# Kernel tuning notes

Measured on AMD Instinct MI355X. Metric: run time of the kernel, lower is better.

## Reference

```python
import jax, jax.numpy as jnp
import numpy as np

BUCKET_BINS = np.array([0, 1, 2, 3, 4, 5, 7, 8, 15, 16, 31, 32, 63, 64], dtype=np.int32)
MAX_WINDOW = 8  # args.span_maximum_length


def _span_index_table(L):
    # Static enumeration of all spans of width 1..MAX_WINDOW (stride-1 unfold).
    starts, ends = [], []
    for w in range(1, min(L, MAX_WINDOW) + 1):
        s = np.arange(0, L - w + 1)
        starts.append(s)
        ends.append(s + w)
    return (np.concatenate(starts).astype(np.int32),
            np.concatenate(ends).astype(np.int32))


def _bucket(width):
    # index of last bin with width >= bin value
    return jnp.searchsorted(jnp.asarray(BUCKET_BINS), width, side='right') - 1


def _fnn(h, W1, b1, W2, b2, W3, b3):
    # Linear->ReLU->(Dropout: eval identity)->Linear->ReLU->Linear->Softmax
    h = jax.nn.relu(h @ W1 + b1)
    h = jax.nn.relu(h @ W2 + b2)
    return jax.nn.softmax(h @ W3 + b3, axis=-1)


def setup_inputs() -> dict:
    key = jax.random.key(0)
    ks = jax.random.split(key, 16)
    B, L, D = 8, 256, 768
    H, WD, DD = 1024, 25, 25
    span_dim = 2 * D + WD          # 1561
    pair_dim = 2 * span_dim + DD   # 3147
    f = jnp.float32

    def g(k, shape, scale):
        return jax.random.normal(k, shape, dtype=f) * scale

    return {
        'x': g(ks[0], (B, L, D), 1.0),
        'width_emb': g(ks[1], (len(BUCKET_BINS), WD), 0.02),
        'dist_emb': g(ks[2], (len(BUCKET_BINS), DD), 0.02),
        'Ws1': g(ks[3], (span_dim, H), 0.02), 'bs1': jnp.zeros((H,), f),
        'Ws2': g(ks[4], (H, H), 0.02), 'bs2': jnp.zeros((H,), f),
        'Ws3': g(ks[5], (H, 3), 0.02), 'bs3': jnp.zeros((3,), f),
        'Wp1': g(ks[6], (pair_dim, H), 0.02), 'bp1': jnp.zeros((H,), f),
        'Wp2': g(ks[7], (H, H), 0.02), 'bp2': jnp.zeros((H,), f),
        'Wp3': g(ks[8], (H, 4), 0.02), 'bp3': jnp.zeros((4,), f),
        'nz': 64,
    }


def reference(x, width_emb, dist_emb, Ws1, bs1, Ws2, bs2, Ws3, bs3,
              Wp1, bp1, Wp2, bp2, Wp3, bp3, nz):
    B, L, D = x.shape
    starts_np, ends_np = _span_index_table(L)
    starts = jnp.asarray(starts_np)
    ends = jnp.asarray(ends_np)

    # ---- SpanRepresentation: [start token, end token, width bucket emb] ----
    w_emb = width_emb[_bucket(ends - starts)]                     # [S, WD]
    spans = jnp.concatenate([
        x[:, starts_np, :],                                       # [B,S,D]
        x[:, ends_np - 1, :],                                     # [B,S,D]
        jnp.broadcast_to(w_emb, (B,) + w_emb.shape),              # [B,S,WD]
    ], axis=-1)                                                   # [B,S,span_dim]

    # ---- span_fnn + PrunedTargetOpinion (top-k on aspect/opinion probs) ----
    span_prob = _fnn(spans, Ws1, bs1, Ws2, bs2, Ws3, bs3)         # [B,S,3]
    _, t_idx = jax.lax.top_k(span_prob[:, :, 1], nz)              # aspect  [B,nz]
    _, o_idx = jax.lax.top_k(span_prob[:, :, 2], nz)              # opinion [B,nz]

    # ---- PairRepresentation: all target x opinion pairs ----
    t_rep = jnp.take_along_axis(spans, t_idx[:, :, None], axis=1) # [B,nz,sd]
    o_rep = jnp.take_along_axis(spans, o_idx[:, :, None], axis=1)
    ta, tb = starts[t_idx], ends[t_idx]                           # [B,nz]
    oc, od = starts[o_idx], ends[o_idx]
    # min_distance(a,b,c,d) = min(|b-c|, |a-d|)
    dist = jnp.minimum(jnp.abs(tb[:, :, None] - oc[:, None, :]),
                       jnp.abs(ta[:, :, None] - od[:, None, :]))  # [B,nz,nz]
    d_emb = dist_emb[_bucket(dist)]                               # [B,nz,nz,DD]
    sd = spans.shape[-1]
    pairs = jnp.concatenate([
        jnp.broadcast_to(t_rep[:, :, None, :], (B, nz, nz, sd)),
        jnp.broadcast_to(o_rep[:, None, :, :], (B, nz, nz, sd)),
        d_emb,
    ], axis=-1).reshape(B, nz * nz, 2 * sd + d_emb.shape[-1])     # [B,nz^2,pair_dim]

    pair_prob = _fnn(pairs, Wp1, bp1, Wp2, bp2, Wp3, bp3)         # [B,nz^2,4]
    return span_prob, pair_prob
```

## Files before the change

### kernel.cpp

```cpp
#include <hip/hip_runtime.h>
#include <cstdint>
#include <cstddef>

#define BATCH 8
#define SEQ   256
#define DIM   768
#define NSPAN 2020
#define HID   1024
#define NZ    64

typedef unsigned short u16;
typedef unsigned int   u32;
typedef unsigned long long u64;

typedef __bf16 bf16x8 __attribute__((ext_vector_type(8)));
typedef float  f32x4  __attribute__((ext_vector_type(4)));

__device__ __forceinline__ u16 f2bf(float f) {
    union { float f; u32 u; } x; x.f = f;
    u32 r = x.u + 0x7fffu + ((x.u >> 16) & 1u);
    return (u16)(r >> 16);
}
__device__ __forceinline__ float bf2f(u16 b) {
    union { u32 u; float f; } x; x.u = ((u32)b) << 16;
// ... 58 lines not shown
    }
    if (bid < 6296) {
        int t = bid - 6144;
        int row = t >> 2;
        int h = (t & 3) * 256 + tid;
        const int wb[8] = {1,2,3,4,5,5,6,7};
        if (row < 8) {
            int bk = wb[row];
            float acc = bs1[h];
            for (int j = 0; j < 25; ++j) acc = fmaf(wemb[bk*25+j], Ws1[(size_t)(1536+j)*HID + h], acc);
            wtabS[row*HID + h] = acc;
        } else if (row < 16) {
            int bk = wb[row-8];
            float acc = 0.f;
            for (int j = 0; j < 25; ++j) acc = fmaf(wemb[bk*25+j], Wp1[(size_t)(1536+j)*HID + h], acc);
            wtabPt[(row-8)*HID + h] = acc;
        } else if (row < 24) {
            int bk = wb[row-16];
            float acc = 0.f;
            for (int j = 0; j < 25; ++j) acc = fmaf(wemb[bk*25+j], Wp1[(size_t)(3097+j)*HID + h], acc);
            wtabPo[(row-16)*HID + h] = acc;
        } else {
            int tt = row - 24;
            float acc = bp1[h];
            for (int j = 0; j < 25; ++j) acc = fmaf(demb[tt*25+j], Wp1[(size_t)(3122+j)*HID + h], acc);
            dtab[tt*HID + h] = acc;
        }
        return;
    }
    const int tb = bid - 6296;
    const int tr = tid >> 3;
    const int tc4 = (tid & 7) * 4;
    int job, tk, tn, blk = 0;
    if (tb < 1536)      { job = 0; tk = tb % 24; tn = tb / 24; }
    else if (tb < 2560) { job = 1; int t = tb - 1536; tk = t & 31; tn = t >> 5; }
    else if (tb < 3584) { job = 2; int t = tb - 2560; tk = t & 31; tn = t >> 5; }
    else                { job = 3; int t = tb - 3584; blk = t / 768; int r = t - blk * 768; tk = r % 24; tn = r / 24; }
    const int k0 = tk * 32, n0 = tn * 32;

    int k = k0 + tr;
    float4 v;
    if (job == 0) {
        const float* s = (n0 < 1024) ? (Ws1 + (size_t)k * HID + n0)
                                     : (Ws1 + (size_t)(768 + k) * HID + (n0 - 1024));
        v = *(const float4*)(s + tc4);
    } else if (job == 1) {
        v = *(const float4*)(Ws2 + (size_t)k * HID + n0 + tc4);
    } else if (job == 2) {
        v = *(const float4*)(Wp2 + (size_t)k * HID + n0 + tc4);
    } else {
        const int roff[4] = {0, 768, 1561, 2329};
        v = *(const float4*)(Wp1 + (size_t)(roff[blk] + k) * HID + n0 + tc4);
    }
    tile[tr][tc4+0] = v.x; tile[tr][tc4+1] = v.y;
    tile[tr][tc4+2] = v.z; tile[tr][tc4+3] = v.w;
    __syncthreads();

    int nn = n0 + tr;
    float w0 = tile[tc4+0][tr], w1 = tile[tc4+1][tr];
    float w2 = tile[tc4+2][tr], w3 = tile[tc4+3][tr];
    if (job == 0) {
        size_t d = (size_t)nn * 768 + k0 + tc4;
        u16 h0,l0,h1,l1,h2,l2,h3,l3;
        splitbf(w0,h0,l0); splitbf(w1,h1,l1); splitbf(w2,h2,l2); splitbf(w3,h3,l3);
        *(uint2*)(W1Th + d) = make_uint2((u32)h0 | ((u32)h1 << 16), (u32)h2 | ((u32)h3 << 16));
        *(uint2*)(W1Tl + d) = make_uint2((u32)l0 | ((u32)l1 << 16), (u32)l2 | ((u32)l3 << 16));
    } else if (job == 1) {
        size_t d = (size_t)nn * 1024 + k0 + tc4;
        u16 h0,l0,h1,l1,h2,l2,h3,l3;
        splitbf(w0,h0,l0); splitbf(w1,h1,l1); splitbf(w2,h2,l2); splitbf(w3,h3,l3);
        *(uint2*)(W2Th + d) = make_uint2((u32)h0 | ((u32)h1 << 16), (u32)h2 | ((u32)h3 << 16));
        *(uint2*)(W2Tl + d) = make_uint2((u32)l0 | ((u32)l1 << 16), (u32)l2 | ((u32)l3 << 16));
    } else if (job == 2) {
        size_t d = (size_t)nn * 1024 + k0 + tc4;
        *(uint2*)(Wp2T + d) = make_uint2((u32)f2bf(w0) | ((u32)f2bf(w1) << 16),
                                         (u32)f2bf(w2) | ((u32)f2bf(w3) << 16));
    } else {
        size_t d = (size_t)blk * 786432 + (size_t)nn * 768 + k0 + tc4;
        *(uint2*)(Wp1T4 + d) = make_uint2((u32)f2bf(w0) | ((u32)f2bf(w1) << 16),
                                          (u32)f2bf(w2) | ((u32)f2bf(w3) << 16));
    }
}

__global__ __launch_bounds__(256) void k_gemm3bf(
    const u16* __restrict__ Ah, const u16* __restrict__ Al, int lda,
    const u16* __restrict__ BTh, const u16* __restrict__ BTl, int ldb,
    float* __restrict__ C, int ldc,
    int M, int K, int nby, int sft)
{
    int bx, by;
    xcd_map(blockIdx.x, sft, bx, by);
    if (by >= nby) return;
    __shared__ __align__(16) u16 sm[2 * 16384];
    const int tid = threadIdx.x;
    const int bm = by * 128, bn = bx * 128;
    const int wave = tid >> 6, lane = tid & 63;
    const int wr = wave >> 1, wc = wave & 1;
    const int q = lane >> 4, tl = lane & 15;

    f32x4 zero = {0.f, 0.f, 0.f, 0.f};
    f32x4 acc[4][4];
#pragma unroll
    for (int i = 0; i < 4; ++i)
#pragma unroll
        for (int j = 0; j < 4; ++j) acc[i][j] = zero;

    const int srow = lane >> 2;
    const int scol = (lane & 3) * 8;
    int ra0 = bm + wave * 32 + srow;      if (ra0 >= M) ra0 = M - 1;
    int ra1 = bm + wave * 32 + 16 + srow; if (ra1 >= M) ra1 = M - 1;
    const int rb0 = bn + wave * 32 + srow;
    const int rb1 = bn + wave * 32 + 16 + srow;
    const u32 oA0 = wave * 1024,          oA1 = oA0 + 512;
    const u32 oL0 = 4096 + wave * 1024,   oL1 = oL0 + 512;
    const u32 oB0 = 8192 + wave * 1024,   oB1 = oB0 + 512;
    const u32 oC0 = 12288 + wave * 1024,  oC1 = oC0 + 512;
    const u16* gA0 = Ah  + (size_t)ra0 * lda + scol;
    const u16* gA1 = Ah  + (size_t)ra1 * lda + scol;
    const u16* gL0 = Al  + (size_t)ra0 * lda + scol;
    const u16* gL1 = Al  + (size_t)ra1 * lda + scol;
    const u16* gB0 = BTh + (size_t)rb0 * ldb + scol;
    const u16* gB1 = BTh + (size_t)rb1 * ldb + scol;
    const u16* gC0 = BTl + (size_t)rb0 * ldb + scol;
    const u16* gC1 = BTl + (size_t)rb1 * ldb + scol;

    gld_lds16(gA0, sm + oA0); gld_lds16(gA1, sm + oA1);
    gld_lds16(gL0, sm + oL0); gld_lds16(gL1, sm + oL1);
    gld_lds16(gB0, sm + oB0); gld_lds16(gB1, sm + oB1);
    gld_lds16(gC0, sm + oC0); gld_lds16(gC1, sm + oC1);
    asm volatile("s_waitcnt vmcnt(0)" ::: "memory");
    asm volatile("s_barrier" ::: "memory");

    const int NT = K >> 5;
    for (int kt = 0; kt < NT; ++kt) {
        const u16* smr = sm + ((kt & 1) ? 16384u : 0u);
        u16*       smw = sm + ((kt & 1) ? 0u : 16384u);
        if (kt < NT - 1) {
            const int k0 = (kt + 1) * 32;
            gld_lds16(gA0 + k0, smw + oA0); gld_lds16(gA1 + k0, smw + oA1);
            gld_lds16(gL0 + k0, smw + oL0); gld_lds16(gL1 + k0, smw + oL1);
            gld_lds16(gB0 + k0, smw + oB0); gld_lds16(gB1 + k0, smw + oB1);
            gld_lds16(gC0 + k0, smw + oC0); gld_lds16(gC1 + k0, smw + oC1);
            asm volatile("s_waitcnt vmcnt(8)" ::: "memory");
        } else {
            asm volatile("s_waitcnt vmcnt(0)" ::: "memory");
        }
        asm volatile("s_barrier" ::: "memory");
        bf16x8 ah[4], al[4], bh[4], bl[4];
#pragma unroll
        for (int t = 0; t < 4; ++t) {
            int arow = (wr*64 + t*16 + tl) * 32 + q*8;
            int brow = (wc*64 + t*16 + tl) * 32 + q*8;
            ah[t] = *(const bf16x8*)(smr + arow);
            al[t] = *(const bf16x8*)(smr + 4096 + arow);
            bh[t] = *(const bf16x8*)(smr + 8192 + brow);
            bl[t] = *(const bf16x8*)(smr + 12288 + brow);
        }
#pragma unroll
        for (int ti = 0; ti < 4; ++ti)
#pragma unroll
            for (int tj = 0; tj < 4; ++tj) {
                acc[ti][tj] = __builtin_amdgcn_mfma_f32_16x16x32_bf16(ah[ti], bh[tj], acc[ti][tj], 0, 0, 0);
                acc[ti][tj] = __builtin_amdgcn_mfma_f32_16x16x32_bf16(al[ti], bh[tj], acc[ti][tj], 0, 0, 0);
                acc[ti][tj] = __builtin_amdgcn_mfma_f32_16x16x32_bf16(ah[ti], bl[tj], acc[ti][tj], 0, 0, 0);
            }
        asm volatile("s_barrier" ::: "memory");
    }
#pragma unroll
    for (int ti = 0; ti < 4; ++ti) {
#pragma unroll
        for (int tj = 0; tj < 4; ++tj) {
            int gcol = bn + wc*64 + tj*16 + tl;
#pragma unroll
            for (int r = 0; r < 4; ++r) {
                int grow = bm + wr*64 + ti*16 + q*4 + r;
                if (grow >= M) continue;
                C[(size_t)grow * ldc + gcol] = acc[ti][tj][r];
            }
        }
    }
}

#define MFB __builtin_amdgcn_mfma_f32_16x16x32_bf16
#define MFROW(i, A, B) \
    acc[i][0] = MFB(A, B[0], acc[i][0], 0, 0, 0); \
    acc[i][1] = MFB(A, B[1], acc[i][1], 0, 0, 0); \
    acc[i][2] = MFB(A, B[2], acc[i][2], 0, 0, 0); \
    acc[i][3] = MFB(A, B[3], acc[i][3], 0, 0, 0);

__global__ __launch_bounds__(512, 2) void k_span_l2(
    const u16* __restrict__ Ah, const u16* __restrict__ Al,
    const u16* __restrict__ BTh, const u16* __restrict__ BTl,
    const float* __restrict__ bs2, const float* __restrict__ Ws3,
    float* __restrict__ part, int M)
{
    __shared__ __align__(16) u16 sm[65536];
    const int tid = threadIdx.x;
    const int swz = (blockIdx.x & 7) * 32 + (blockIdx.x >> 3);
    const int by = swz >> 2, bx = swz & 3;
    const int bm = by * 256, bn = bx * 256;
    const int wave = tid >> 6, lane = tid & 63;
    const int wm = wave >> 2, wn = wave & 3;
    const int tl = lane & 15, q8 = lane >> 4;

    const int sr  = lane >> 2;
    const int scs = lane & 3;
    const int scl = scs ^ ((sr >> 1) & 3);
    const u16* gsrc[8];
    u32 ldst[8];
#pragma unroll
    for (int c = 0; c < 4; ++c) {
        int arr  = 2 + (c >> 1);
        int half = c & 1;
        int sb   = wave;
        int row  = bn + half * 128 + sb * 16 + sr;
        const u16* base = (arr == 2) ? BTh : BTl;
        gsrc[c] = base + (size_t)row * HID + scl * 8;
        ldst[c] = arr * 8192 + half * 4096 + sb * 512;
    }
#pragma unroll
    for (int p = 0; p < 4; ++p) {
        int arr  = wave >> 2;
        int half = (wave >> 1) & 1;
        int sb   = 2 * p + (wave & 1);
        int row  = bm + half * 128 + sb * 16 + sr;
        if (row >= M) row = M - 1;
        const u16* base = arr ? Al : Ah;
        gsrc[4 + p] = base + (size_t)row * HID + scl * 8;
        ldst[4 + p] = arr * 8192 + half * 4096 + sb * 512;
    }
    const int cpr = q8 ^ ((tl >> 1) & 3);
    const u32 lof = (u32)(tl * 32 + cpr * 8);
    const u32 rA  = (u32)(wm * 4096) + lof;
    const u32 rB  = 16384u + (u32)((wn >> 1) * 4096 + (wn & 1) * 2048) + lof;

    f32x4 zero = {0.f, 0.f, 0.f, 0.f};
    f32x4 acc[8][4];
#pragma unroll
    for (int i = 0; i < 8; ++i)
#pragma unroll
        for (int j = 0; j < 4; ++j) acc[i][j] = zero;

#pragma unroll
    for (int c = 0; c < 8; ++c) gld_lds16(gsrc[c], sm + ldst[c]);
    asm volatile("s_waitcnt vmcnt(3)" ::: "memory");
    asm volatile("s_barrier" ::: "memory");

    bf16x8 bh[4], bl[4];
    bf16x8 aXh0, aXh1, aXl0, aXl1, aYh0, aYh1, aYl0, aYl1;
#pragma unroll
    for (int fn = 0; fn < 4; ++fn) {
        bh[fn] = *(const bf16x8*)(sm + rB + fn * 512);
        bl[fn] = *(const bf16x8*)(sm + rB + 8192 + fn * 512);
    }
    aXh0 = *(const bf16x8*)(sm + rA + 0 * 512);
    aXh1 = *(const bf16x8*)(sm + rA + 1 * 512);
    aXl0 = *(const bf16x8*)(sm + rA + 8192 + 0 * 512);
    aXl1 = *(const bf16x8*)(sm + rA + 8192 + 1 * 512);

    for (int t = 0; t < 32; ++t) {
        const u16* smr = sm + ((t & 1) ? 32768u : 0u);
        u16*       smw = sm + ((t & 1) ? 0u : 32768u);
        const int  kn  = (t + 1) * 32;
        gld_lds16(gsrc[0] + kn, smw + ldst[0]);
        gld_lds16(gsrc[1] + kn, smw + ldst[1]);
        gld_lds16(gsrc[2] + kn, smw + ldst[2]);
        asm volatile("s_waitcnt vmcnt(5)" ::: "memory");
        asm volatile("s_barrier" ::: "memory");
        __builtin_amdgcn_sched_barrier(0);
        __builtin_amdgcn_s_setprio(1);
        MFROW(0, aXh0, bh) MFROW(1, aXh1, bh)
        aYh0 = *(const bf16x8*)(smr + rA + 2 * 512);
        aYh1 = *(const bf16x8*)(smr + rA + 3 * 512);
        aYl0 = *(const bf16x8*)(smr + rA + 8192 + 2 * 512);
        aYl1 = *(const bf16x8*)(smr + rA + 8192 + 3 * 512);
        MFROW(0, aXl0, bh) MFROW(1, aXl1, bh)
        MFROW(0, aXh0, bl) MFROW(1, aXh1, bl)
        __builtin_amdgcn_s_setprio(0);
        gld_lds16(gsrc[3] + kn, smw + ldst[3]);
        gld_lds16(gsrc[4] + kn, smw + ldst[4]);
        asm volatile("s_waitcnt vmcnt(6)" ::: "memory");
        asm volatile("s_barrier" ::: "memory");
        __builtin_amdgcn_sched_barrier(0);
        __builtin_amdgcn_s_setprio(1);
        MFROW(2, aYh0, bh) MFROW(3, aYh1, bh)
        aXh0 = *(const bf16x8*)(smr + rA + 4 * 512);
        aXh1 = *(const bf16x8*)(smr + rA + 5 * 512);
        aXl0 = *(const bf16x8*)(smr + rA + 8192 + 4 * 512);
        aXl1 = *(const bf16x8*)(smr + rA + 8192 + 5 * 512);
        MFROW(2, aYl0, bh) MFROW(3, aYl1, bh)
        MFROW(2, aYh0, bl) MFROW(3, aYh1, bl)
        __builtin_amdgcn_s_setprio(0);
        gld_lds16(gsrc[5] + kn, smw + ldst[5]);
        gld_lds16(gsrc[6] + kn, smw + ldst[6]);
        asm volatile("s_waitcnt vmcnt(7)" ::: "memory");
        asm volatile("s_barrier" ::: "memory");
        __builtin_amdgcn_sched_barrier(0);
        __builtin_amdgcn_s_setprio(1);
        MFROW(4, aXh0, bh) MFROW(5, aXh1, bh)
        aYh0 = *(const bf16x8*)(smr + rA + 6 * 512);
        aYh1 = *(const bf16x8*)(smr + rA + 7 * 512);
        aYl0 = *(const bf16x8*)(smr + rA + 8192 + 6 * 512);
        aYl1 = *(const bf16x8*)(smr + rA + 8192 + 7 * 512);
        MFROW(4, aXl0, bh) MFROW(5, aXl1, bh)
        MFROW(4, aXh0, bl) MFROW(5, aXh1, bl)
        __builtin_amdgcn_s_setprio(0);
        gld_lds16(gsrc[7] + kn, smw + ldst[7]);
        asm volatile("s_waitcnt vmcnt(3)" ::: "memory");
        asm volatile("s_barrier" ::: "memory");
        __builtin_amdgcn_sched_barrier(0);
        __builtin_amdgcn_s_setprio(1);
        MFROW(6, aYh0, bh) MFROW(7, aYh1, bh)
        aXh0 = *(const bf16x8*)(smw + rA + 0 * 512);
        aXh1 = *(const bf16x8*)(smw + rA + 1 * 512);
        aXl0 = *(const bf16x8*)(smw + rA + 8192 + 0 * 512);
        aXl1 = *(const bf16x8*)(smw + rA + 8192 + 1 * 512);
        MFROW(6, aYl0, bh) MFROW(7, aYl1, bh)
        MFROW(6, aYh0, bl) MFROW(7, aYh1, bl)
        __builtin_amdgcn_s_setprio(0);
#pragma unroll
        for (int fn = 0; fn < 4; ++fn) {
            bh[fn] = *(const bf16x8*)(smw + rB + fn * 512);
            bl[fn] = *(const bf16x8*)(smw + rB + 8192 + fn * 512);
        }
        asm volatile("s_barrier" ::: "memory");
    }

    const int slot = bx * 4 + wn;
#pragma unroll
    for (int fm = 0; fm < 8; ++fm) {
#pragma unroll
        for (int r = 0; r < 4; ++r) {
            int grow = bm + wm * 128 + fm * 16 + q8 * 4 + r;
            float l0 = 0.f, l1 = 0.f, l2 = 0.f;
#pragma unroll
            for (int fn = 0; fn < 4; ++fn) {
                int gcol = bn + wn * 64 + fn * 16 + tl;
                float v = fmaxf(acc[fm][fn][r] + bs2[gcol], 0.f);
                const float* w3 = Ws3 + gcol * 3;
                l0 = fmaf(v, w3[0], l0);
                l1 = fmaf(v, w3[1], l1);
                l2 = fmaf(v, w3[2], l2);
            }
#pragma unroll
            for (int off = 8; off > 0; off >>= 1) {
                l0 += __shfl_down(l0, off, 16);
                l1 += __shfl_down(l1, off, 16);
                l2 += __shfl_down(l2, off, 16);
            }
            if (tl == 0 && grow < M) {
                float* dst = part + ((size_t)grow * 16 + slot) * 3;
                dst[0] = l0; dst[1] = l1; dst[2] = l2;
            }
        }
    }
    asm volatile("s_waitcnt vmcnt(0)" ::: "memory");
}

__global__ __launch_bounds__(256) void k_pairL1(
    const u16* __restrict__ xh, const u16* __restrict__ Wp1T4,
    float* __restrict__ TO2, const int* __restrict__ toks)
{
    __shared__ __align__(16) u16 sm[2 * 4096];
    const int tid = threadIdx.x;
    const int bid = blockIdx.x;
    const int p = bid >> 8;
    const int bx = bid & 15, by = (bid >> 4) & 15;
    const int bm = by * 64, bn = bx * 64;
    const int wave = tid >> 6, lane = tid & 63;
    const int wr = wave >> 1, wc = wave & 1;
    const int q = lane >> 4, tl = lane & 15;
    const bool isO = bm >= 512;

    f32x4 zero = {0.f, 0.f, 0.f, 0.f};
    f32x4 acc[2][2];
#pragma unroll
    for (int i = 0; i < 2; ++i)
#pragma unroll
        for (int j = 0; j < 2; ++j) acc[i][j] = zero;

    const int srow = tid >> 2;
    const int scol = (tid & 3) * 8;
    const u32 oA = wave * 512;
    const u32 oB = 2048 + wave * 512;

    int arow = toks[bm + srow + p * 1024];
    const u16* gA = xh + (size_t)arow * DIM + scol;
    const u16* gB = Wp1T4 + ((size_t)((isO ? 2 : 0) + p) * 1024 + bn + srow) * DIM + scol;

    gld_lds16(gA, sm + oA);
    gld_lds16(gB, sm + oB);
    asm volatile("s_waitcnt vmcnt(0)" ::: "memory");
    asm volatile("s_barrier" ::: "memory");

    const int NT = DIM / 32;
    for (int kt = 0; kt < NT; ++kt) {
        const u16* smr = sm + ((kt & 1) ? 4096u : 0u);
        u16*       smw = sm + ((kt & 1) ? 0u : 4096u);
        if (kt < NT - 1) {
            const int k0 = (kt + 1) * 32;
            gld_lds16(gA + k0, smw + oA);
            gld_lds16(gB + k0, smw + oB);
// ... 106 lines not shown
    if (tid < NZ) {
        u64 key = keys[tid];
        int fi = (int)(0xFFFFFFFFu - (u32)(key & 0xFFFFFFFFu));
        if (fi < 0 || fi >= NSPAN) fi = 0;
        outp[tid] = fi;
        int st, en, w; span_decode(fi, st, en, w);
        int base = (head == 1 ? 0 : 512) + b * NZ + tid;
        toks[base] = b * SEQ + st;
        toks[1024 + base] = b * SEQ + en - 1;
    }
}

__global__ __launch_bounds__(256) void k_build_h1p(
    const float* __restrict__ TO2, const int* __restrict__ t_idx, const int* __restrict__ o_idx,
    const float* __restrict__ wtabPt, const float* __restrict__ wtabPo,
    const float* __restrict__ dtab, u16* __restrict__ h1p)
{
    __shared__ float Ts[8][HID];
    __shared__ float Os[4][HID];
    const int bid = blockIdx.x;
    const int b = bid >> 7;
    const int it = (bid >> 4) & 7;
    const int jt = bid & 15;
    const int i0 = it * 8, j0 = jt * 4;
    const int tid = threadIdx.x;
    const int k4 = tid * 4;
    const size_t PS = (size_t)1024 * HID;

    int tinfo[8][2];
    int oinfo[4][2];
#pragma unroll
    for (int r = 0; r < 8; ++r) {
        int i = i0 + r;
        int ts = t_idx[b*64 + i];
        int ta, tb, wt; span_decode(ts, ta, tb, wt);
        tinfo[r][0] = ta; tinfo[r][1] = tb;
        float4 t0 = *(const float4*)(TO2 + (size_t)(b*64 + i) * HID + k4);
        float4 t1 = *(const float4*)(TO2 + PS + (size_t)(b*64 + i) * HID + k4);
        float4 pp = *(const float4*)(wtabPt + (size_t)(wt-1) * HID + k4);
        Ts[r][k4+0] = t0.x + t1.x + pp.x;
        Ts[r][k4+1] = t0.y + t1.y + pp.y;
        Ts[r][k4+2] = t0.z + t1.z + pp.z;
        Ts[r][k4+3] = t0.w + t1.w + pp.w;
    }
#pragma unroll
    for (int r = 0; r < 4; ++r) {
        int j = j0 + r;
        int os = o_idx[b*64 + j];
        int oc, od, wo; span_decode(os, oc, od, wo);
        oinfo[r][0] = oc; oinfo[r][1] = od;
        float4 o0 = *(const float4*)(TO2 + (size_t)(512 + b*64 + j) * HID + k4);
        float4 o1 = *(const float4*)(TO2 + PS + (size_t)(512 + b*64 + j) * HID + k4);
        float4 qq = *(const float4*)(wtabPo + (size_t)(wo-1) * HID + k4);
        Os[r][k4+0] = o0.x + o1.x + qq.x;
        Os[r][k4+1] = o0.y + o1.y + qq.y;
        Os[r][k4+2] = o0.z + o1.z + qq.z;
        Os[r][k4+3] = o0.w + o1.w + qq.w;
    }
    __syncthreads();

#pragma unroll
    for (int ri = 0; ri < 8; ++ri) {
#pragma unroll
        for (int rj = 0; rj < 4; ++rj) {
            int ta = tinfo[ri][0], tb = tinfo[ri][1];
            int oc = oinfo[rj][0], od = oinfo[rj][1];
            int d1 = tb - oc; d1 = d1 < 0 ? -d1 : d1;
            int d2 = ta - od; d2 = d2 < 0 ? -d2 : d2;
            int dist = d1 < d2 ? d1 : d2;
            int db = dbucket(dist);
            const float4 dd = *(const float4*)(dtab + (size_t)db * HID + k4);
            float vx = fmaxf(Ts[ri][k4+0] + Os[rj][k4+0] + dd.x, 0.f);
            float vy = fmaxf(Ts[ri][k4+1] + Os[rj][k4+1] + dd.y, 0.f);
            float vz = fmaxf(Ts[ri][k4+2] + Os[rj][k4+2] + dd.z, 0.f);
            float vw = fmaxf(Ts[ri][k4+3] + Os[rj][k4+3] + dd.w, 0.f);
            u32 p0 = (u32)f2bf(vx) | ((u32)f2bf(vy) << 16);
            u32 p1 = (u32)f2bf(vz) | ((u32)f2bf(vw) << 16);
            int row = b * 4096 + (i0 + ri) * 64 + (j0 + rj);
            *(uint2*)(h1p + (size_t)row * HID + k4) = make_uint2(p0, p1);
        }
    }
}

__global__ __launch_bounds__(512, 2) void k_pair_l2(
    const u16* __restrict__ Abf, const u16* __restrict__ BT,
    const float* __restrict__ bp2, const float* __restrict__ Wp3,
    float* __restrict__ part)
{
    __shared__ __align__(16) u16 sm[65536];
    const int tid = threadIdx.x;
    const int swz = (blockIdx.x & 7) * 64 + (blockIdx.x >> 3);
    const int by = swz >> 2, bx = swz & 3;
    const int bm = by * 256, bn = bx * 256;
    const int wave = tid >> 6, lane = tid & 63;
    const int wm = wave >> 2, wn = wave & 3;
    const int tl = lane & 15, q8 = lane >> 4;

    const int sr  = lane >> 2;
    const int scs = lane & 3;
    const int scl = scs ^ ((sr >> 1) & 3);
    const u16* gsrc[8];
    u32 ldst[8];
#pragma unroll
    for (int c = 0; c < 4; ++c) {
        int half = c >> 1;
        int sb   = (c & 1) * 8 + wave;
        int row  = bn + half * 128 + (sb >> 1) * 16 + sr;
        gsrc[c] = BT + (size_t)row * HID + (sb & 1) * 32 + scl * 8;
        ldst[c] = 16384 + half * 8192 + sb * 512;
    }
#pragma unroll
    for (int p = 0; p < 4; ++p) {
        int half = wave >> 2;
        int sb   = 4 * p + (wave & 3);
        int row  = bm + half * 128 + (sb >> 1) * 16 + sr;
        gsrc[4 + p] = Abf + (size_t)row * HID + (sb & 1) * 32 + scl * 8;
        ldst[4 + p] = half * 8192 + sb * 512;
    }
    const int cpr = q8 ^ ((tl >> 1) & 3);
    const u32 lof = (u32)(tl * 32 + cpr * 8);
    const u32 rA  = (u32)(wm * 8192) + lof;
    const u32 rB  = 16384u + (u32)((wn >> 1) * 8192 + (wn & 1) * 4096) + lof;

    f32x4 zero = {0.f, 0.f, 0.f, 0.f};
    f32x4 acc[8][4];
#pragma unroll
    for (int i = 0; i < 8; ++i)
#pragma unroll
        for (int j = 0; j < 4; ++j) acc[i][j] = zero;

#pragma unroll
    for (int c = 0; c < 8; ++c) gld_lds16(gsrc[c], sm + ldst[c]);
    asm volatile("s_waitcnt vmcnt(3)" ::: "memory");
    asm volatile("s_barrier" ::: "memory");

    bf16x8 b0[4], b1[4];
    bf16x8 xa00, xa01, xa10, xa11, ya00, ya01, ya10, ya11;
#pragma unroll
    for (int fn = 0; fn < 4; ++fn) {
        b0[fn] = *(const bf16x8*)(sm + rB + (fn * 2 + 0) * 512);
        b1[fn] = *(const bf16x8*)(sm + rB + (fn * 2 + 1) * 512);
    }
    xa00 = *(const bf16x8*)(sm + rA + 0 * 512);
    xa01 = *(const bf16x8*)(sm + rA + 1 * 512);
    xa10 = *(const bf16x8*)(sm + rA + 2 * 512);
    xa11 = *(const bf16x8*)(sm + rA + 3 * 512);

    for (int t = 0; t < 16; ++t) {
        const u16* smr = sm + ((t & 1) ? 32768u : 0u);
        u16*       smw = sm + ((t & 1) ? 0u : 32768u);
        const int  kn  = (t + 1) * 64;
        gld_lds16(gsrc[0] + kn, smw + ldst[0]);
        gld_lds16(gsrc[1] + kn, smw + ldst[1]);
        gld_lds16(gsrc[2] + kn, smw + ldst[2]);
        asm volatile("s_waitcnt vmcnt(5)" ::: "memory");
        asm volatile("s_barrier" ::: "memory");
        __builtin_amdgcn_sched_barrier(0);
        __builtin_amdgcn_s_setprio(1);
        MFROW(0, xa00, b0) MFROW(1, xa10, b0)
        ya00 = *(const bf16x8*)(smr + rA + 4 * 512);
        ya01 = *(const bf16x8*)(smr + rA + 5 * 512);
        ya10 = *(const bf16x8*)(smr + rA + 6 * 512);
        ya11 = *(const bf16x8*)(smr + rA + 7 * 512);
        MFROW(0, xa01, b1) MFROW(1, xa11, b1)
        __builtin_amdgcn_s_setprio(0);
        gld_lds16(gsrc[3] + kn, smw + ldst[3]);
        gld_lds16(gsrc[4] + kn, smw + ldst[4]);
        asm volatile("s_waitcnt vmcnt(6)" ::: "memory");
        asm volatile("s_barrier" ::: "memory");
        __builtin_amdgcn_sched_barrier(0);
        __builtin_amdgcn_s_setprio(1);
        MFROW(2, ya00, b0) MFROW(3, ya10, b0)
        xa00 = *(const bf16x8*)(smr + rA + 8 * 512);
        xa01 = *(const bf16x8*)(smr + rA + 9 * 512);
        xa10 = *(const bf16x8*)(smr + rA + 10 * 512);
        xa11 = *(const bf16x8*)(smr + rA + 11 * 512);
        MFROW(2, ya01, b1) MFROW(3, ya11, b1)
        __builtin_amdgcn_s_setprio(0);
        gld_lds16(gsrc[5] + kn, smw + ldst[5]);
        gld_lds16(gsrc[6] + kn, smw + ldst[6]);
        asm volatile("s_waitcnt vmcnt(7)" ::: "memory");
        asm volatile("s_barrier" ::: "memory");
        __builtin_amdgcn_sched_barrier(0);
        __builtin_amdgcn_s_setprio(1);
        MFROW(4, xa00, b0) MFROW(5, xa10, b0)
        ya00 = *(const bf16x8*)(smr + rA + 12 * 512);
        ya01 = *(const bf16x8*)(smr + rA + 13 * 512);
        ya10 = *(const bf16x8*)(smr + rA + 14 * 512);
        ya11 = *(const bf16x8*)(smr + rA + 15 * 512);
        MFROW(4, xa01, b1) MFROW(5, xa11, b1)
        __builtin_amdgcn_s_setprio(0);
        gld_lds16(gsrc[7] + kn, smw + ldst[7]);
        asm volatile("s_waitcnt vmcnt(3)" ::: "memory");
        asm volatile("s_barrier" ::: "memory");
        __builtin_amdgcn_sched_barrier(0);
        __builtin_amdgcn_s_setprio(1);
        MFROW(6, ya00, b0) MFROW(7, ya10, b0)
        xa00 = *(const bf16x8*)(smw + rA + 0 * 512);
        xa01 = *(const bf16x8*)(smw + rA + 1 * 512);
        xa10 = *(const bf16x8*)(smw + rA + 2 * 512);
        xa11 = *(const bf16x8*)(smw + rA + 3 * 512);
        MFROW(6, ya01, b1) MFROW(7, ya11, b1)
        __builtin_amdgcn_s_setprio(0);
#pragma unroll
        for (int fn = 0; fn < 4; ++fn) {
            b0[fn] = *(const bf16x8*)(smw + rB + (fn * 2 + 0) * 512);
            b1[fn] = *(const bf16x8*)(smw + rB + (fn * 2 + 1) * 512);
        }
        asm volatile("s_barrier" ::: "memory");
    }

    const int slot = bx * 4 + wn;
#pragma unroll
    for (int fm = 0; fm < 8; ++fm) {
#pragma unroll
        for (int r = 0; r < 4; ++r) {
            int grow = bm + wm * 128 + fm * 16 + q8 * 4 + r;
            float l0 = 0.f, l1 = 0.f, l2 = 0.f, l3 = 0.f;
#pragma unroll
            for (int fn = 0; fn < 4; ++fn) {
                int gcol = bn + wn * 64 + fn * 16 + tl;
                float v = fmaxf(acc[fm][fn][r] + bp2[gcol], 0.f);
                const float4 w = *(const float4*)(Wp3 + gcol * 4);
                l0 = fmaf(v, w.x, l0); l1 = fmaf(v, w.y, l1);
                l2 = fmaf(v, w.z, l2); l3 = fmaf(v, w.w, l3);
            }
#pragma unroll
            for (int off = 8; off > 0; off >>= 1) {
                l0 += __shfl_down(l0, off, 16);
                l1 += __shfl_down(l1, off, 16);
                l2 += __shfl_down(l2, off, 16);
                l3 += __shfl_down(l3, off, 16);
            }
            if (tl == 0) {
                float* dst = part + ((size_t)grow * 16 + slot) * 4;
                dst[0] = l0; dst[1] = l1; dst[2] = l2; dst[3] = l3;
            }
        }
    }
    asm volatile("s_waitcnt vmcnt(0)" ::: "memory");
}

__global__ __launch_bounds__(256) void k_pair_red(
    const float* __restrict__ part, const float* __restrict__ bp3,
    float* __restrict__ out)
{
    int r = blockIdx.x * 256 + threadIdx.x;
    const float4* p = (const float4*)(part + (size_t)r * 64);
    float s0 = bp3[0], s1 = bp3[1], s2 = bp3[2], s3 = bp3[3];
#pragma unroll
    for (int t = 0; t < 16; ++t) {
        float4 v = p[t];
        s0 += v.x; s1 += v.y; s2 += v.z; s3 += v.w;
    }
    float m = fmaxf(fmaxf(s0, s1), fmaxf(s2, s3));
    float e0 = expf(s0 - m), e1 = expf(s1 - m), e2 = expf(s2 - m), e3 = expf(s3 - m);
    float inv = 1.f / (e0 + e1 + e2 + e3);
    float* o = out + (size_t)r * 4;
    o[0] = e0 * inv; o[1] = e1 * inv; o[2] = e2 * inv; o[3] = e3 * inv;
}

extern "C" void kernel_launch(void* const* d_in, const int* in_sizes, int n_in,
                              void* d_out, int out_size, void* d_ws, size_t ws_size,
                              hipStream_t stream)
{
    const float* x    = (const float*)d_in[0];
    const float* wemb = (const float*)d_in[1];
    const float* demb = (const float*)d_in[2];
    const float* Ws1  = (const float*)d_in[3];
    const float* bs1  = (const float*)d_in[4];
    const float* Ws2  = (const float*)d_in[5];
    const float* bs2  = (const float*)d_in[6];
    const float* Ws3  = (const float*)d_in[7];
    const float* bs3  = (const float*)d_in[8];
    const float* Wp1  = (const float*)d_in[9];
    const float* bp1  = (const float*)d_in[10];
    const float* Wp2  = (const float*)d_in[11];
    const float* bp2  = (const float*)d_in[12];
    const float* Wp3  = (const float*)d_in[13];
    const float* bp3  = (const float*)d_in[14];
    float* out = (float*)d_out;
    char* ws = (char*)d_ws;

    const size_t RSZ = (size_t)32768 * HID * 2;
    size_t off = 0;
    auto alloc = [&](size_t bytes) -> void* {
        void* p = ws + off;
        off += (bytes + 255) & ~(size_t)255;
        return p;
    };
    char* R1 = (char*)alloc(RSZ);
    char* R2 = (char*)alloc(RSZ);
    u16*   h1h  = (u16*)R1;
    u16*   h1l  = (u16*)(R1 + (size_t)16160 * HID * 2);
    float* XALL = (float*)R2;
    u16*   xl   = (u16*)(R2 + (16u << 20));
    u16*   W1Th = (u16*)(R2 + (19u << 20));
    u16*   W1Tl = (u16*)(R2 + (22u << 20));
    u16*   h1p  = (u16*)R2;
    u16*   xh     = (u16*)alloc((size_t)2048 * DIM * 2);
    float* TO2    = (float*)alloc((size_t)2 * 1024 * HID * 4);
    float* partS  = (float*)alloc((size_t)16160 * 16 * 3 * 4);
    float* partP  = (float*)alloc((size_t)32768 * 16 * 4 * 4);
    u16*   W2Th   = (u16*)alloc((size_t)1024 * 1024 * 2);
    u16*   W2Tl   = (u16*)alloc((size_t)1024 * 1024 * 2);
    u16*   Wp2T   = (u16*)alloc((size_t)1024 * 1024 * 2);
    u16*   Wp1T4  = (u16*)alloc((size_t)4 * 1024 * 768 * 2);
    float* wtabS  = (float*)alloc(8 * HID * 4);
    float* wtabPt = (float*)alloc(8 * HID * 4);
    float* wtabPo = (float*)alloc(8 * HID * 4);
    float* dtab   = (float*)alloc(14 * HID * 4);
    int*   t_idx  = (int*)alloc(BATCH * NZ * 4);
    int*   o_idx  = (int*)alloc(BATCH * NZ * 4);
    int*   toks   = (int*)alloc(2048 * 4);
    (void)ws_size; (void)in_sizes; (void)n_in; (void)out_size;

    k_prep<<<12952, 256, 0, stream>>>(x, xh, xl, wemb, demb, bs1, bp1,
                                      wtabS, wtabPt, wtabPo, dtab,
                                      Ws1, W1Th, W1Tl, Ws2, W2Th, W2Tl,
                                      Wp2, Wp2T, Wp1, Wp1T4);

    k_gemm3bf<<<256, 256, 0, stream>>>(xh, xl, 768, W1Th, W1Tl, 768,
                                       XALL, 2048, 2048, 768, 16, 4);
    k_build_h1s<<<16160, 256, 0, stream>>>(XALL, wtabS, h1h, h1l);
    k_span_l2<<<256, 512, 0, stream>>>(h1h, h1l, W2Th, W2Tl, bs2, Ws3, partS, 16160);
    k_topk<<<16, 1024, 0, stream>>>(partS, bs3, out, t_idx, o_idx, toks);
    k_pairL1<<<512, 256, 0, stream>>>(xh, Wp1T4, TO2, toks);
    k_build_h1p<<<1024, 256, 0, stream>>>(TO2, t_idx, o_idx, wtabPt, wtabPo, dtab, h1p);
    k_pair_l2<<<512, 512, 0, stream>>>(h1p, Wp2T, bp2, Wp3, partP);
    k_pair_red<<<128, 256, 0, stream>>>(partP, bp3, out + 48480);
}
```

Before: 457.6 us.

## Rework GEMM kernels: 8-wave gemm3bf with swizzled LDS, restructured l2 pipelines

k_gemm3bf moves from 4 to 8 waves per block, with each wave owning a 64x32 output tile. Global-to-LDS loads are split by array across wave pairs and use an XOR-swizzled column layout to cut LDS bank conflicts. In k_span_l2, the A-fragment LDS reads now come after all MFMAs of a phase instead of being interleaved with them, fenced by sched barriers. In k_pair_l2, the hand-unrolled register double-buffered phases become a macro that loads fragments at the start of each phase and adds an extra barrier, trading load/compute overlap for lower register pressure and simpler code.

```diff
diff --git a/kernel.cpp b/kernel.cpp
--- a/kernel.cpp
+++ b/kernel.cpp
@@ -164,7 +164,14 @@
     }
 }
 
-__global__ __launch_bounds__(256) void k_gemm3bf(
+#define MFB __builtin_amdgcn_mfma_f32_16x16x32_bf16
+#define MFROW(i, A, B) \
+    acc[i][0] = MFB(A, B[0], acc[i][0], 0, 0, 0); \
+    acc[i][1] = MFB(A, B[1], acc[i][1], 0, 0, 0); \
+    acc[i][2] = MFB(A, B[2], acc[i][2], 0, 0, 0); \
+    acc[i][3] = MFB(A, B[3], acc[i][3], 0, 0, 0);
+
+__global__ __launch_bounds__(512) void k_gemm3bf(
     const u16* __restrict__ Ah, const u16* __restrict__ Al, int lda,
     const u16* __restrict__ BTh, const u16* __restrict__ BTl, int ldb,
     float* __restrict__ C, int ldc,
@@ -177,39 +184,37 @@
     const int tid = threadIdx.x;
     const int bm = by * 128, bn = bx * 128;
     const int wave = tid >> 6, lane = tid & 63;
-    const int wr = wave >> 1, wc = wave & 1;
-    const int q = lane >> 4, tl = lane & 15;
+    const int wr = wave >> 2, wc = wave & 3;
+    const int q8 = lane >> 4, tl = lane & 15;
 
     f32x4 zero = {0.f, 0.f, 0.f, 0.f};
-    f32x4 acc[4][4];
+    f32x4 acc[4][2];
 #pragma unroll
     for (int i = 0; i < 4; ++i)
 #pragma unroll
-        for (int j = 0; j < 4; ++j) acc[i][j] = zero;
-
-    const int srow = lane >> 2;
-    const int scol = (lane & 3) * 8;
-    int ra0 = bm + wave * 32 + srow;      if (ra0 >= M) ra0 = M - 1;
-    int ra1 = bm + wave * 32 + 16 + srow; if (ra1 >= M) ra1 = M - 1;
-    const int rb0 = bn + wave * 32 + srow;
-    const int rb1 = bn + wave * 32 + 16 + srow;
-    const u32 oA0 = wave * 1024,          oA1 = oA0 + 512;
-    const u32 oL0 = 4096 + wave * 1024,   oL1 = oL0 + 512;
-    const u32 oB0 = 8192 + wave * 1024,   oB1 = oB0 + 512;
-    const u32 oC0 = 12288 + wave * 1024,  oC1 = oC0 + 512;
-    const u16* gA0 = Ah  + (size_t)ra0 * lda + scol;
-    const u16* gA1 = Ah  + (size_t)ra1 * lda + scol;
-    const u16* gL0 = Al  + (size_t)ra0 * lda + scol;
-    const u16* gL1 = Al  + (size_t)ra1 * lda + scol;
-    const u16* gB0 = BTh + (size_t)rb0 * ldb + scol;
-    const u16* gB1 = BTh + (size_t)rb1 * ldb + scol;
-    const u16* gC0 = BTl + (size_t)rb0 * ldb + scol;
-    const u16* gC1 = BTl + (size_t)rb1 * ldb + scol;
-
-    gld_lds16(gA0, sm + oA0); gld_lds16(gA1, sm + oA1);
-    gld_lds16(gL0, sm + oL0); gld_lds16(gL1, sm + oL1);
-    gld_lds16(gB0, sm + oB0); gld_lds16(gB1, sm + oB1);
-    gld_lds16(gC0, sm + oC0); gld_lds16(gC1, sm + oC1);
+        for (int j = 0; j < 2; ++j) acc[i][j] = zero;
+
+    const int arr  = wave >> 1;
+    const int half = wave & 1;
+    const int sr   = lane >> 2;
+    const int scs  = lane & 3;
+    const int scl  = scs ^ ((sr >> 1) & 3);
+    const u16* gsrc[4];
+    u32 ldst[4];
+#pragma unroll
+    for (int j = 0; j < 4; ++j) {
+        int row = ((arr < 2) ? bm : bn) + half * 64 + j * 16 + sr;
+        if (arr < 2 && row >= M) row = M - 1;
+        const u16* base = (arr == 0) ? Ah : (arr == 1) ? Al : (arr == 2) ? BTh : BTl;
+        int ld = (arr < 2) ? lda : ldb;
+        gsrc[j] = base + (size_t)row * ld + scl * 8;
+        ldst[j] = arr * 4096 + half * 2048 + j * 512;
+    }
+    const int cpr = q8 ^ ((tl >> 1) & 3);
+    const u32 lof = (u32)(tl * 32 + cpr * 8);
+
+#pragma unroll
+    for (int j = 0; j < 4; ++j) gld_lds16(gsrc[j], sm + ldst[j]);
     asm volatile("s_waitcnt vmcnt(0)" ::: "memory");
     asm volatile("s_barrier" ::: "memory");
 
@@ -219,56 +224,49 @@
         u16*       smw = sm + ((kt & 1) ? 0u : 16384u);
         if (kt < NT - 1) {
             const int k0 = (kt + 1) * 32;
-            gld_lds16(gA0 + k0, smw + oA0); gld_lds16(gA1 + k0, smw + oA1);
-            gld_lds16(gL0 + k0, smw + oL0); gld_lds16(gL1 + k0, smw + oL1);
-            gld_lds16(gB0 + k0, smw + oB0); gld_lds16(gB1 + k0, smw + oB1);
-            gld_lds16(gC0 + k0, smw + oC0); gld_lds16(gC1 + k0, smw + oC1);
-            asm volatile("s_waitcnt vmcnt(8)" ::: "memory");
+#pragma unroll
+            for (int j = 0; j < 4; ++j) gld_lds16(gsrc[j] + k0, smw + ldst[j]);
+            asm volatile("s_waitcnt vmcnt(4)" ::: "memory");
         } else {
             asm volatile("s_waitcnt vmcnt(0)" ::: "memory");
         }
         asm volatile("s_barrier" ::: "memory");
-        bf16x8 ah[4], al[4], bh[4], bl[4];
-#pragma unroll
-        for (int t = 0; t < 4; ++t) {
-            int arow = (wr*64 + t*16 + tl) * 32 + q*8;
-            int brow = (wc*64 + t*16 + tl) * 32 + q*8;
-            ah[t] = *(const bf16x8*)(smr + arow);
-            al[t] = *(const bf16x8*)(smr + 4096 + arow);
-            bh[t] = *(const bf16x8*)(smr + 8192 + brow);
-            bl[t] = *(const bf16x8*)(smr + 12288 + brow);
-        }
-#pragma unroll
-        for (int ti = 0; ti < 4; ++ti)
-#pragma unroll
-            for (int tj = 0; tj < 4; ++tj) {
-                acc[ti][tj] = __builtin_amdgcn_mfma_f32_16x16x32_bf16(ah[ti], bh[tj], acc[ti][tj], 0, 0, 0);
-                acc[ti][tj] = __builtin_amdgcn_mfma_f32_16x16x32_bf16(al[ti], bh[tj], acc[ti][tj], 0, 0, 0);
-                acc[ti][tj] = __builtin_amdgcn_mfma_f32_16x16x32_bf16(ah[ti], bl[tj], acc[ti][tj], 0, 0, 0);
+        __builtin_amdgcn_sched_barrier(0);
+        bf16x8 ah[4], al[4], bh[2], bl[2];
+#pragma unroll
+        for (int fm = 0; fm < 4; ++fm) {
+            ah[fm] = *(const bf16x8*)(smr + (wr*4 + fm) * 512 + lof);
+            al[fm] = *(const bf16x8*)(smr + 4096 + (wr*4 + fm) * 512 + lof);
+        }
+#pragma unroll
+        for (int fn = 0; fn < 2; ++fn) {
+            bh[fn] = *(const bf16x8*)(smr + 8192 + (wc*2 + fn) * 512 + lof);
+            bl[fn] = *(const bf16x8*)(smr + 12288 + (wc*2 + fn) * 512 + lof);
+        }
+#pragma unroll
+        for (int fm = 0; fm < 4; ++fm)
+#pragma unroll
+            for (int fn = 0; fn < 2; ++fn) {
+                acc[fm][fn] = MFB(ah[fm], bh[fn], acc[fm][fn], 0, 0, 0);
+                acc[fm][fn] = MFB(al[fm], bh[fn], acc[fm][fn], 0, 0, 0);
+                acc[fm][fn] = MFB(ah[fm], bl[fn], acc[fm][fn], 0, 0, 0);
             }
         asm volatile("s_barrier" ::: "memory");
     }
 #pragma unroll
-    for (int ti = 0; ti < 4; ++ti) {
-#pragma unroll
-        for (int tj = 0; tj < 4; ++tj) {
-            int gcol = bn + wc*64 + tj*16 + tl;
+    for (int fm = 0; fm < 4; ++fm) {
+#pragma unroll
+        for (int fn = 0; fn < 2; ++fn) {
+            int gcol = bn + wc*32 + fn*16 + tl;
 #pragma unroll
             for (int r = 0; r < 4; ++r) {
-                int grow = bm + wr*64 + ti*16 + q*4 + r;
+                int grow = bm + wr*64 + fm*16 + q8*4 + r;
                 if (grow >= M) continue;
-                C[(size_t)grow * ldc + gcol] = acc[ti][tj][r];
-            }
-        }
-    }
-}
-
-#define MFB __builtin_amdgcn_mfma_f32_16x16x32_bf16
-#define MFROW(i, A, B) \
-    acc[i][0] = MFB(A, B[0], acc[i][0], 0, 0, 0); \
-    acc[i][1] = MFB(A, B[1], acc[i][1], 0, 0, 0); \
-    acc[i][2] = MFB(A, B[2], acc[i][2], 0, 0, 0); \
-    acc[i][3] = MFB(A, B[3], acc[i][3], 0, 0, 0);
+                C[(size_t)grow * ldc + gcol] = acc[fm][fn][r];
+            }
+        }
+    }
+}
 
 __global__ __launch_bounds__(512, 2) void k_span_l2(
     const u16* __restrict__ Ah, const u16* __restrict__ Al,
@@ -352,13 +350,14 @@
         __builtin_amdgcn_sched_barrier(0);
         __builtin_amdgcn_s_setprio(1);
         MFROW(0, aXh0, bh) MFROW(1, aXh1, bh)
+        MFROW(0, aXl0, bh) MFROW(1, aXl1, bh)
+        MFROW(0, aXh0, bl) MFROW(1, aXh1, bl)
+        __builtin_amdgcn_s_setprio(0);
+        __builtin_amdgcn_sched_barrier(0);
         aYh0 = *(const bf16x8*)(smr + rA + 2 * 512);
         aYh1 = *(const bf16x8*)(smr + rA + 3 * 512);
         aYl0 = *(const bf16x8*)(smr + rA + 8192 + 2 * 512);
         aYl1 = *(const bf16x8*)(smr + rA + 8192 + 3 * 512);
-        MFROW(0, aXl0, bh) MFROW(1, aXl1, bh)
-        MFROW(0, aXh0, bl) MFROW(1, aXh1, bl)
-        __builtin_amdgcn_s_setprio(0);
         gld_lds16(gsrc[3] + kn, smw + ldst[3]);
         gld_lds16(gsrc[4] + kn, smw + ldst[4]);
         asm volatile("s_waitcnt vmcnt(6)" ::: "memory");
@@ -366,13 +365,14 @@
         __builtin_amdgcn_sched_barrier(0);
         __builtin_amdgcn_s_setprio(1);
         MFROW(2, aYh0, bh) MFROW(3, aYh1, bh)
+        MFROW(2, aYl0, bh) MFROW(3, aYl1, bh)
+        MFROW(2, aYh0, bl) MFROW(3, aYh1, bl)
+        __builtin_amdgcn_s_setprio(0);
+        __builtin_amdgcn_sched_barrier(0);
         aXh0 = *(const bf16x8*)(smr + rA + 4 * 512);
         aXh1 = *(const bf16x8*)(smr + rA + 5 * 512);
         aXl0 = *(const bf16x8*)(smr + rA + 8192 + 4 * 512);
         aXl1 = *(const bf16x8*)(smr + rA + 8192 + 5 * 512);
-        MFROW(2, aYl0, bh) MFROW(3, aYl1, bh)
-        MFROW(2, aYh0, bl) MFROW(3, aYh1, bl)
-        __builtin_amdgcn_s_setprio(0);
         gld_lds16(gsrc[5] + kn, smw + ldst[5]);
         gld_lds16(gsrc[6] + kn, smw + ldst[6]);
         asm volatile("s_waitcnt vmcnt(7)" ::: "memory");
@@ -380,26 +380,28 @@
         __builtin_amdgcn_sched_barrier(0);
         __builtin_amdgcn_s_setprio(1);
         MFROW(4, aXh0, bh) MFROW(5, aXh1, bh)
+        MFROW(4, aXl0, bh) MFROW(5, aXl1, bh)
+        MFROW(4, aXh0, bl) MFROW(5, aXh1, bl)
+        __builtin_amdgcn_s_setprio(0);
+        __builtin_amdgcn_sched_barrier(0);
         aYh0 = *(const bf16x8*)(smr + rA + 6 * 512);
         aYh1 = *(const bf16x8*)(smr + rA + 7 * 512);
         aYl0 = *(const bf16x8*)(smr + rA + 8192 + 6 * 512);
         aYl1 = *(const bf16x8*)(smr + rA + 8192 + 7 * 512);
-        MFROW(4, aXl0, bh) MFROW(5, aXl1, bh)
-        MFROW(4, aXh0, bl) MFROW(5, aXh1, bl)
-        __builtin_amdgcn_s_setprio(0);
         gld_lds16(gsrc[7] + kn, smw + ldst[7]);
         asm volatile("s_waitcnt vmcnt(3)" ::: "memory");
         asm volatile("s_barrier" ::: "memory");
         __builtin_amdgcn_sched_barrier(0);
         __builtin_amdgcn_s_setprio(1);
         MFROW(6, aYh0, bh) MFROW(7, aYh1, bh)
+        MFROW(6, aYl0, bh) MFROW(7, aYl1, bh)
+        MFROW(6, aYh0, bl) MFROW(7, aYh1, bl)
+        __builtin_amdgcn_s_setprio(0);
+        __builtin_amdgcn_sched_barrier(0);
         aXh0 = *(const bf16x8*)(smw + rA + 0 * 512);
         aXh1 = *(const bf16x8*)(smw + rA + 1 * 512);
         aXl0 = *(const bf16x8*)(smw + rA + 8192 + 0 * 512);
         aXl1 = *(const bf16x8*)(smw + rA + 8192 + 1 * 512);
-        MFROW(6, aYl0, bh) MFROW(7, aYl1, bh)
-        MFROW(6, aYh0, bl) MFROW(7, aYh1, bl)
-        __builtin_amdgcn_s_setprio(0);
 #pragma unroll
         for (int fn = 0; fn < 4; ++fn) {
             bh[fn] = *(const bf16x8*)(smw + rB + fn * 512);
@@ -672,6 +674,35 @@
     }
 }
 
+#define PAIR_PHASE(P, VMC, GLDS) \
+    { \
+        bf16x8 a00 = *(const bf16x8*)(smr + rA + ((2*(P)+0)*2+0)*512); \
+        bf16x8 a01 = *(const bf16x8*)(smr + rA + ((2*(P)+0)*2+1)*512); \
+        bf16x8 a10 = *(const bf16x8*)(smr + rA + ((2*(P)+1)*2+0)*512); \
+        bf16x8 a11 = *(const bf16x8*)(smr + rA + ((2*(P)+1)*2+1)*512); \
+        if ((P) == 0) { \
+            b0[0] = *(const bf16x8*)(smr + rB + 0*512); \
+            b1[0] = *(const bf16x8*)(smr + rB + 1*512); \
+            b0[1] = *(const bf16x8*)(smr + rB + 2*512); \
+            b1[1] = *(const bf16x8*)(smr + rB + 3*512); \
+            b0[2] = *(const bf16x8*)(smr + rB + 4*512); \
+            b1[2] = *(const bf16x8*)(smr + rB + 5*512); \
+            b0[3] = *(const bf16x8*)(smr + rB + 6*512); \
+            b1[3] = *(const bf16x8*)(smr + rB + 7*512); \
+        } \
+        GLDS \
+        asm volatile("s_waitcnt vmcnt(" #VMC ")" ::: "memory"); \
+        asm volatile("s_barrier" ::: "memory"); \
+        __builtin_amdgcn_sched_barrier(0); \
+        __builtin_amdgcn_s_setprio(1); \
+        MFROW(2*(P)+0, a00, b0) \
+        MFROW(2*(P)+1, a10, b0) \
+        MFROW(2*(P)+0, a01, b1) \
+        MFROW(2*(P)+1, a11, b1) \
+        __builtin_amdgcn_s_setprio(0); \
+        asm volatile("s_barrier" ::: "memory"); \
+    }
+
 __global__ __launch_bounds__(512, 2) void k_pair_l2(
     const u16* __restrict__ Abf, const u16* __restrict__ BT,
     const float* __restrict__ bp2, const float* __restrict__ Wp3,
@@ -725,79 +756,22 @@
     asm volatile("s_barrier" ::: "memory");
 
     bf16x8 b0[4], b1[4];
-    bf16x8 xa00, xa01, xa10, xa11, ya00, ya01, ya10, ya11;
-#pragma unroll
-    for (int fn = 0; fn < 4; ++fn) {
-        b0[fn] = *(const bf16x8*)(sm + rB + (fn * 2 + 0) * 512);
-        b1[fn] = *(const bf16x8*)(sm + rB + (fn * 2 + 1) * 512);
-    }
-    xa00 = *(const bf16x8*)(sm + rA + 0 * 512);
-    xa01 = *(const bf16x8*)(sm + rA + 1 * 512);
-    xa10 = *(const bf16x8*)(sm + rA + 2 * 512);
-    xa11 = *(const bf16x8*)(sm + rA + 3 * 512);
-
     for (int t = 0; t < 16; ++t) {
         const u16* smr = sm + ((t & 1) ? 32768u : 0u);
         u16*       smw = sm + ((t & 1) ? 0u : 32768u);
         const int  kn  = (t + 1) * 64;
-        gld_lds16(gsrc[0] + kn, smw + ldst[0]);
-        gld_lds16(gsrc[1] + kn, smw + ldst[1]);
-        gld_lds16(gsrc[2] + kn, smw + ldst[2]);
-        asm volatile("s_waitcnt vmcnt(5)" ::: "memory");
-        asm volatile("s_barrier" ::: "memory");
-        __builtin_amdgcn_sched_barrier(0);
-        __builtin_amdgcn_s_setprio(1);
-        MFROW(0, xa00, b0) MFROW(1, xa10, b0)
-        ya00 = *(const bf16x8*)(smr + rA + 4 * 512);
-        ya01 = *(const bf16x8*)(smr + rA + 5 * 512);
-        ya10 = *(const bf16x8*)(smr + rA + 6 * 512);
-        ya11 = *(const bf16x8*)(smr + rA + 7 * 512);
-        MFROW(0, xa01, b1) MFROW(1, xa11, b1)
-        __builtin_amdgcn_s_setprio(0);
-        gld_lds16(gsrc[3] + kn, smw + ldst[3]);
-        gld_lds16(gsrc[4] + kn, smw + ldst[4]);
-        asm volatile("s_waitcnt vmcnt(6)" ::: "memory");
-        asm volatile("s_barrier" ::: "memory");
-        __builtin_amdgcn_sched_barrier(0);
-        __builtin_amdgcn_s_setprio(1);
-        MFROW(2, ya00, b0) MFROW(3, ya10, b0)
-        xa00 = *(const bf16x8*)(smr + rA + 8 * 512);
-        xa01 = *(const bf16x8*)(smr + rA + 9 * 512);
-        xa10 = *(const bf16x8*)(smr + rA + 10 * 512);
-        xa11 = *(const bf16x8*)(smr + rA + 11 * 512);
-        MFROW(2, ya01, b1) MFROW(3, ya11, b1)
-        __builtin_amdgcn_s_setprio(0);
-        gld_lds16(gsrc[5] + kn, smw + ldst[5]);
-        gld_lds16(gsrc[6] + kn, smw + ldst[6]);
-        asm volatile("s_waitcnt vmcnt(7)" ::: "memory");
-        asm volatile("s_barrier" ::: "memory");
-        __builtin_amdgcn_sched_barrier(0);
-        __builtin_amdgcn_s_setprio(1);
-        MFROW(4, xa00, b0) MFROW(5, xa10, b0)
-        ya00 = *(const bf16x8*)(smr + rA + 12 * 512);
-        ya01 = *(const bf16x8*)(smr + rA + 13 * 512);
-        ya10 = *(const bf16x8*)(smr + rA + 14 * 512);
-        ya11 = *(const bf16x8*)(smr + rA + 15 * 512);
-        MFROW(4, xa01, b1) MFROW(5, xa11, b1)
-        __builtin_amdgcn_s_setprio(0);
-        gld_lds16(gsrc[7] + kn, smw + ldst[7]);
-        asm volatile("s_waitcnt vmcnt(3)" ::: "memory");
-        asm volatile("s_barrier" ::: "memory");
-        __builtin_amdgcn_sched_barrier(0);
-        __builtin_amdgcn_s_setprio(1);
-        MFROW(6, ya00, b0) MFROW(7, ya10, b0)
-        xa00 = *(const bf16x8*)(smw + rA + 0 * 512);
-        xa01 = *(const bf16x8*)(smw + rA + 1 * 512);
-        xa10 = *(const bf16x8*)(smw + rA + 2 * 512);
-        xa11 = *(const bf16x8*)(smw + rA + 3 * 512);
-        MFROW(6, ya01, b1) MFROW(7, ya11, b1)
-        __builtin_amdgcn_s_setprio(0);
-#pragma unroll
-        for (int fn = 0; fn < 4; ++fn) {
-            b0[fn] = *(const bf16x8*)(smw + rB + (fn * 2 + 0) * 512);
-            b1[fn] = *(const bf16x8*)(smw + rB + (fn * 2 + 1) * 512);
-        }
-        asm volatile("s_barrier" ::: "memory");
+        PAIR_PHASE(0, 5,
+            gld_lds16(gsrc[0] + kn, smw + ldst[0]);
+            gld_lds16(gsrc[1] + kn, smw + ldst[1]);
+            gld_lds16(gsrc[2] + kn, smw + ldst[2]);)
+        PAIR_PHASE(1, 6,
+            gld_lds16(gsrc[3] + kn, smw + ldst[3]);
+            gld_lds16(gsrc[4] + kn, smw + ldst[4]);)
+        PAIR_PHASE(2, 7,
+            gld_lds16(gsrc[5] + kn, smw + ldst[5]);
+            gld_lds16(gsrc[6] + kn, smw + ldst[6]);)
+        PAIR_PHASE(3, 3,
+            gld_lds16(gsrc[7] + kn, smw + ldst[7]);)
     }
 
     const int slot = bx * 4 + wn;
@@ -910,7 +884,7 @@
                                       Ws1, W1Th, W1Tl, Ws2, W2Th, W2Tl,
                                       Wp2, Wp2T, Wp1, Wp1T4);
 
-    k_gemm3bf<<<256, 256, 0, stream>>>(xh, xl, 768, W1Th, W1Tl, 768,
+    k_gemm3bf<<<256, 512, 0, stream>>>(xh, xl, 768, W1Th, W1Tl, 768,
                                        XALL, 2048, 2048, 768, 16, 4);
     k_build_h1s<<<16160, 256, 0, stream>>>(XALL, wtabS, h1h, h1l);
     k_span_l2<<<256, 512, 0, stream>>>(h1h, h1l, W2Th, W2Tl, bs2, Ws3, partS, 16160);
```

Result: faster. 386.9 us (-15.4%).
